# Kernel optimization log

Measured on AMD Instinct MI355X. Metric: run time of the kernel, lower is better.

The kernel has to match this reference:

```python
import jax, jax.numpy as jnp
import numpy as np

EPS_NORM = 1e-12
EPS_ABS = 1e-12


def _stack3(x):
    # x: [B, T, C] -> [B, T, 3, C] with left-shift, identity, right-shift taps
    prev = jnp.pad(x[:, :-1, :], ((0, 0), (1, 0), (0, 0)))
    nxt = jnp.pad(x[:, 1:, :], ((0, 0), (0, 1), (0, 0)))
    return jnp.stack([prev, x, nxt], axis=2)


def _l2_norm(x, axis):
    # matches layer's l2_normal: sqrt(max(sum(x^2), eps)), keepdims
    sq = jnp.sum(jnp.square(x), axis=axis, keepdims=True)
    return jnp.sqrt(jnp.maximum(sq, EPS_NORM))


def setup_inputs() -> dict:
    key = jax.random.key(0)
    k1, k2 = jax.random.split(key)
    B, T, C, K, U = 32, 4096, 128, 3, 256
    inputs = jax.random.normal(k1, (B, T, C), dtype=jnp.float32)
    # glorot uniform for w: limit = sqrt(6/(fan_in+fan_out)) with fan_in=C*K, fan_out=U
    limit = np.sqrt(6.0 / (C * K + U)).astype(np.float32)
    w = jax.random.uniform(k2, (1, C * K, U), dtype=jnp.float32, minval=-limit, maxval=limit)
    b = jnp.zeros((U,), dtype=jnp.float32)
    p = jnp.ones((U,), dtype=jnp.float32)
    q = jnp.zeros((1,), dtype=jnp.float32)
    return {"inputs": inputs, "w": w, "b": b, "p": p, "q": q}


def reference(inputs, w, b, p, q):
    B, T, C = inputs.shape
    U = w.shape[-1]
    x = _stack3(inputs).reshape(B, T, 3 * C)          # [B, T, 3C] (tap-major, matches tf stack+reshape)
    q2 = jnp.square(q)                                 # [1]
    x_norm = _l2_norm(x, axis=2) + q2                  # [B, T, 1]
    w_norm = _l2_norm(w, axis=1) + q2                  # [1, 1, U]
    w2 = w[0]                                          # [3C, U]
    sign = jnp.sign(jnp.einsum('btk,ku->btu', x, w2))  # sign of raw matmul
    y = jnp.einsum('btk,ku->btu', x / x_norm, w2 / w_norm[0])
    y = jnp.abs(y) + EPS_ABS
    y = jnp.power(y, jnp.square(p))                    # broadcast over units
    y = sign * y + b
    return y
```

## Files before the change

kernel.cpp:

```cpp
#include <hip/hip_runtime.h>

typedef __attribute__((ext_vector_type(8))) short short8;
typedef __attribute__((ext_vector_type(4))) float f32x4;

#define T_DIM 4096
#define C_DIM 128
#define U_DIM 256
#define BM 128
#define NROWS 130
#define LDK 136

__device__ __forceinline__ unsigned short f2bf(float f) {
    unsigned int u = __float_as_uint(f);
    u += 0x7FFFu + ((u >> 16) & 1u);
    return (unsigned short)(u >> 16);
}

__global__ void prep_kernel(const float* __restrict__ w,
                            const float* __restrict__ b,
                            const float* __restrict__ p,
                            const float* __restrict__ q,
                            unsigned short* __restrict__ wfrag,
                            float* __restrict__ winv,
                            float* __restrict__ p2,
                            float* __restrict__ bc) {
    if (blockIdx.x < 48) {
        int idx = blockIdx.x * 256 + threadIdx.x;
        int l  = idx & 63;
        int nt = (idx >> 6) & 15;
        int ks = idx >> 10;
        int n  = nt * 16 + (l & 15);
        int k0 = ks * 32 + ((l >> 4) << 3);
        #pragma unroll
        for (int j = 0; j < 8; ++j) {
            wfrag[(size_t)idx * 8 + j] = f2bf(w[(k0 + j) * U_DIM + n]);
        }
    } else {
        int u = threadIdx.x;
        float ss = 0.f;
        for (int k = 0; k < 3 * C_DIM; ++k) {
            float v = w[k * U_DIM + u];
            ss += v * v;
        }
        float q2 = q[0] * q[0];
        winv[u] = 1.0f / (sqrtf(fmaxf(ss, 1e-12f)) + q2);
        float pv = p[u];
        p2[u] = pv * pv;
        bc[u] = b[u];
    }
}

__global__ __launch_bounds__(512, 4) void cossim_main(
        const float* __restrict__ inp,
        const unsigned short* __restrict__ wfrag,
        const float* __restrict__ winv,
        const float* __restrict__ p2g,
        const float* __restrict__ bg,
        const float* __restrict__ qg,
        float* __restrict__ out) {
    __shared__ unsigned short inp_s[NROWS][LDK];
    __shared__ float ss_s[NROWS];
    __shared__ float xninv_s[BM];

    const int tid  = threadIdx.x;
    const int bidx = blockIdx.x;
    const int bb   = bidx >> 5;
    const int t0   = (bidx & 31) * BM;

    {
        const int r0 = tid >> 5;
        const int lc = (tid & 31) * 4;
        float4 v[9];
        #pragma unroll
        for (int i = 0; i < 9; ++i) {
            int r = r0 + i * 16;
            int t = t0 + r - 1;
            float4 val = make_float4(0.f, 0.f, 0.f, 0.f);
            if (r < NROWS && t >= 0 && t < T_DIM) {
                val = *(const float4*)(inp + ((size_t)bb * T_DIM + t) * C_DIM + lc);
            }
            v[i] = val;
        }
        #pragma unroll
        for (int i = 0; i < 9; ++i) {
            int r = r0 + i * 16;
            if (r < NROWS) {
                float4 val = v[i];
                float part = val.x * val.x + val.y * val.y + val.z * val.z + val.w * val.w;
                #pragma unroll
                for (int o = 16; o > 0; o >>= 1) part += __shfl_xor(part, o, 32);
                if ((tid & 31) == 0) ss_s[r] = part;
                ushort4 sv;
                sv.x = f2bf(val.x); sv.y = f2bf(val.y);
                sv.z = f2bf(val.z); sv.w = f2bf(val.w);
                *(ushort4*)(&inp_s[r][lc]) = sv;
            }
        }
    }
    __syncthreads();
    if (tid < BM) {
        float s3 = ss_s[tid] + ss_s[tid + 1] + ss_s[tid + 2];
        float q2 = qg[0] * qg[0];
        xninv_s[tid] = 1.0f / (sqrtf(fmaxf(s3, 1e-12f)) + q2);
    }
    __syncthreads();

    const int wid = tid >> 6;
    const int l   = tid & 63;
    const int tw  = wid >> 2;
    const int uw  = wid & 3;
    const int l15 = l & 15;
    const int lg  = l >> 4;

    f32x4 acc[4][4];
    #pragma unroll
    for (int tf = 0; tf < 4; ++tf)
        #pragma unroll
        for (int uf = 0; uf < 4; ++uf)
            acc[tf][uf] = (f32x4){0.f, 0.f, 0.f, 0.f};

    const short8* wf = (const short8*)wfrag;

    #pragma unroll
    for (int ks = 0; ks < 12; ++ks) {
        const int tap = ks >> 2;
        const int c0  = (ks & 3) * 32 + lg * 8;
        short8 xv[4], wv[4];
        #pragma unroll
        for (int tf = 0; tf < 4; ++tf) {
            int row = tw * 64 + tf * 16 + l15 + tap;
            xv[tf] = *(const short8*)(&inp_s[row][c0]);
        }
        #pragma unroll
        for (int uf = 0; uf < 4; ++uf) {
            wv[uf] = wf[(size_t)(ks * 16 + uw * 4 + uf) * 64 + l];
        }
        #pragma unroll
        for (int tf = 0; tf < 4; ++tf)
            #pragma unroll
            for (int uf = 0; uf < 4; ++uf)
                acc[tf][uf] = __builtin_amdgcn_mfma_f32_16x16x32_bf16(
                    wv[uf], xv[tf], acc[tf][uf], 0, 0, 0);
    }

    #pragma unroll
    for (int tf = 0; tf < 4; ++tf) {
        int trow = tw * 64 + tf * 16 + l15;
        float xi = xninv_s[trow];
        float* orow = out + ((size_t)bb * T_DIM + t0 + trow) * U_DIM;
        #pragma unroll
        for (int uf = 0; uf < 4; ++uf) {
            int uc = uw * 64 + uf * 16 + lg * 4;
            f32x4 wiv = *(const f32x4*)(winv + uc);
            f32x4 ppv = *(const f32x4*)(p2g + uc);
            f32x4 bbv = *(const f32x4*)(bg + uc);
            f32x4 r;
            #pragma unroll
            for (int j = 0; j < 4; ++j) {
                float raw = acc[tf][uf][j];
                float y   = raw * xi * wiv[j];
                float ay  = fabsf(y) + 1e-12f;
                float pw  = ppv[j];
                float rr  = ay;
                if (pw != 1.0f) rr = powf(ay, pw);
                float s   = (raw > 0.f) ? 1.f : ((raw < 0.f) ? -1.f : 0.f);
                r[j] = s * rr + bbv[j];
            }
            *(f32x4*)(orow + uc) = r;
        }
    }
}

extern "C" void kernel_launch(void* const* d_in, const int* in_sizes, int n_in,
                              void* d_out, int out_size, void* d_ws, size_t ws_size,
                              hipStream_t stream) {
    const float* inp = (const float*)d_in[0];
    const float* w   = (const float*)d_in[1];
    const float* b   = (const float*)d_in[2];
    const float* p   = (const float*)d_in[3];
    const float* q   = (const float*)d_in[4];
    float* out = (float*)d_out;

    unsigned short* wfrag = (unsigned short*)d_ws;
    float* winv = (float*)((char*)d_ws + 196608);
    float* p2   = winv + 256;
    float* bc   = p2 + 256;

    prep_kernel<<<49, 256, 0, stream>>>(w, b, p, q, wfrag, winv, p2, bc);
    cossim_main<<<1024, 512, 0, stream>>>(inp, wfrag, winv, p2, bc, q, out);
}
```

Baseline: 74.01 us.

## Loop over multiple time tiles per block with register-prefetched double-buffered LDS

Each block now processes four 64-row time tiles sequentially instead of one 128-row tile. The next tile's input is loaded into registers during the current tile's MFMA and epilogue, then written to a second LDS buffer. The goal is to overlap global input loads with compute and output stores. In exchange, the grid is halved, halo overhead per tile rises, and the extra barriers add cost.

```diff
diff --git a/kernel.cpp b/kernel.cpp
--- a/kernel.cpp
+++ b/kernel.cpp
@@ -6,9 +6,10 @@
 #define T_DIM 4096
 #define C_DIM 128
 #define U_DIM 256
-#define BM 128
-#define NROWS 130
+#define BM 64
+#define NROWS 66
 #define LDK 136
+#define NT 4
 
 __device__ __forceinline__ unsigned short f2bf(float f) {
     unsigned int u = __float_as_uint(f);
@@ -58,52 +59,15 @@
         const float* __restrict__ bg,
         const float* __restrict__ qg,
         float* __restrict__ out) {
-    __shared__ unsigned short inp_s[NROWS][LDK];
-    __shared__ float ss_s[NROWS];
-    __shared__ float xninv_s[BM];
-
-    const int tid  = threadIdx.x;
-    const int bidx = blockIdx.x;
-    const int bb   = bidx >> 5;
-    const int t0   = (bidx & 31) * BM;
-
-    {
-        const int r0 = tid >> 5;
-        const int lc = (tid & 31) * 4;
-        float4 v[9];
-        #pragma unroll
-        for (int i = 0; i < 9; ++i) {
-            int r = r0 + i * 16;
-            int t = t0 + r - 1;
-            float4 val = make_float4(0.f, 0.f, 0.f, 0.f);
-            if (r < NROWS && t >= 0 && t < T_DIM) {
-                val = *(const float4*)(inp + ((size_t)bb * T_DIM + t) * C_DIM + lc);
-            }
-            v[i] = val;
-        }
-        #pragma unroll
-        for (int i = 0; i < 9; ++i) {
-            int r = r0 + i * 16;
-            if (r < NROWS) {
-                float4 val = v[i];
-                float part = val.x * val.x + val.y * val.y + val.z * val.z + val.w * val.w;
-                #pragma unroll
-                for (int o = 16; o > 0; o >>= 1) part += __shfl_xor(part, o, 32);
-                if ((tid & 31) == 0) ss_s[r] = part;
-                ushort4 sv;
-                sv.x = f2bf(val.x); sv.y = f2bf(val.y);
-                sv.z = f2bf(val.z); sv.w = f2bf(val.w);
-                *(ushort4*)(&inp_s[r][lc]) = sv;
-            }
-        }
-    }
-    __syncthreads();
-    if (tid < BM) {
-        float s3 = ss_s[tid] + ss_s[tid + 1] + ss_s[tid + 2];
-        float q2 = qg[0] * qg[0];
-        xninv_s[tid] = 1.0f / (sqrtf(fmaxf(s3, 1e-12f)) + q2);
-    }
-    __syncthreads();
+    __shared__ unsigned short xs[2][NROWS][LDK];
+    __shared__ float ss_s[2][NROWS];
+
+    const int tid = threadIdx.x;
+    const int bb  = blockIdx.x >> 4;
+    const int tp0 = (blockIdx.x & 15) * NT;
+
+    const int r0 = tid >> 5;
+    const int lc = (tid & 31) * 4;
 
     const int wid = tid >> 6;
     const int l   = tid & 63;
@@ -112,62 +76,139 @@
     const int l15 = l & 15;
     const int lg  = l >> 4;
 
-    f32x4 acc[4][4];
-    #pragma unroll
-    for (int tf = 0; tf < 4; ++tf)
-        #pragma unroll
-        for (int uf = 0; uf < 4; ++uf)
-            acc[tf][uf] = (f32x4){0.f, 0.f, 0.f, 0.f};
-
+    const float q2 = qg[0] * qg[0];
     const short8* wf = (const short8*)wfrag;
 
-    #pragma unroll
-    for (int ks = 0; ks < 12; ++ks) {
-        const int tap = ks >> 2;
-        const int c0  = (ks & 3) * 32 + lg * 8;
-        short8 xv[4], wv[4];
-        #pragma unroll
-        for (int tf = 0; tf < 4; ++tf) {
-            int row = tw * 64 + tf * 16 + l15 + tap;
-            xv[tf] = *(const short8*)(&inp_s[row][c0]);
-        }
-        #pragma unroll
-        for (int uf = 0; uf < 4; ++uf) {
-            wv[uf] = wf[(size_t)(ks * 16 + uw * 4 + uf) * 64 + l];
-        }
-        #pragma unroll
-        for (int tf = 0; tf < 4; ++tf)
+    float4 v[5];
+    {
+        const float* base = inp + (size_t)bb * T_DIM * C_DIM;
+        int t0 = tp0 * BM;
+        #pragma unroll
+        for (int jj = 0; jj < 5; ++jj) {
+            int r = r0 + jj * 16;
+            int t = t0 + r - 1;
+            float4 val = make_float4(0.f, 0.f, 0.f, 0.f);
+            if (r < NROWS && (unsigned)t < T_DIM)
+                val = *(const float4*)(base + (size_t)t * C_DIM + lc);
+            v[jj] = val;
+        }
+        #pragma unroll
+        for (int jj = 0; jj < 5; ++jj) {
+            int r = r0 + jj * 16;
+            if (r < NROWS) {
+                float4 val = v[jj];
+                float part = val.x * val.x + val.y * val.y + val.z * val.z + val.w * val.w;
+                #pragma unroll
+                for (int o = 16; o > 0; o >>= 1) part += __shfl_xor(part, o, 32);
+                if ((tid & 31) == 0) ss_s[0][r] = part;
+                ushort4 sv;
+                sv.x = f2bf(val.x); sv.y = f2bf(val.y);
+                sv.z = f2bf(val.z); sv.w = f2bf(val.w);
+                *(ushort4*)(&xs[0][r][lc]) = sv;
+            }
+        }
+    }
+    __syncthreads();
+
+    int cur = 0;
+    for (int i = 0; i < NT; ++i) {
+        const int t0 = (tp0 + i) * BM;
+
+        float4 vn[5];
+        if (i + 1 < NT) {
+            const float* base = inp + (size_t)bb * T_DIM * C_DIM;
+            int t0n = (tp0 + i + 1) * BM;
+            #pragma unroll
+            for (int jj = 0; jj < 5; ++jj) {
+                int r = r0 + jj * 16;
+                int t = t0n + r - 1;
+                float4 val = make_float4(0.f, 0.f, 0.f, 0.f);
+                if (r < NROWS && (unsigned)t < T_DIM)
+                    val = *(const float4*)(base + (size_t)t * C_DIM + lc);
+                vn[jj] = val;
+            }
+        }
+
+        const unsigned short (*xb)[LDK] = xs[cur];
+        const float* ssb = ss_s[cur];
+
+        f32x4 acc[2][4];
+        #pragma unroll
+        for (int tf = 0; tf < 2; ++tf)
             #pragma unroll
             for (int uf = 0; uf < 4; ++uf)
-                acc[tf][uf] = __builtin_amdgcn_mfma_f32_16x16x32_bf16(
-                    wv[uf], xv[tf], acc[tf][uf], 0, 0, 0);
-    }
-
-    #pragma unroll
-    for (int tf = 0; tf < 4; ++tf) {
-        int trow = tw * 64 + tf * 16 + l15;
-        float xi = xninv_s[trow];
-        float* orow = out + ((size_t)bb * T_DIM + t0 + trow) * U_DIM;
-        #pragma unroll
-        for (int uf = 0; uf < 4; ++uf) {
-            int uc = uw * 64 + uf * 16 + lg * 4;
-            f32x4 wiv = *(const f32x4*)(winv + uc);
-            f32x4 ppv = *(const f32x4*)(p2g + uc);
-            f32x4 bbv = *(const f32x4*)(bg + uc);
-            f32x4 r;
-            #pragma unroll
-            for (int j = 0; j < 4; ++j) {
-                float raw = acc[tf][uf][j];
-                float y   = raw * xi * wiv[j];
-                float ay  = fabsf(y) + 1e-12f;
-                float pw  = ppv[j];
-                float rr  = ay;
-                if (pw != 1.0f) rr = powf(ay, pw);
-                float s   = (raw > 0.f) ? 1.f : ((raw < 0.f) ? -1.f : 0.f);
-                r[j] = s * rr + bbv[j];
-            }
-            *(f32x4*)(orow + uc) = r;
-        }
+                acc[tf][uf] = (f32x4){0.f, 0.f, 0.f, 0.f};
+
+        #pragma unroll
+        for (int ks = 0; ks < 12; ++ks) {
+            const int tap = ks >> 2;
+            const int c0  = (ks & 3) * 32 + lg * 8;
+            short8 xv[2], wv[4];
+            #pragma unroll
+            for (int tf = 0; tf < 2; ++tf) {
+                int row = tw * 32 + tf * 16 + l15 + tap;
+                xv[tf] = *(const short8*)(&xb[row][c0]);
+            }
+            #pragma unroll
+            for (int uf = 0; uf < 4; ++uf) {
+                wv[uf] = wf[(size_t)(ks * 16 + uw * 4 + uf) * 64 + l];
+            }
+            #pragma unroll
+            for (int tf = 0; tf < 2; ++tf)
+                #pragma unroll
+                for (int uf = 0; uf < 4; ++uf)
+                    acc[tf][uf] = __builtin_amdgcn_mfma_f32_16x16x32_bf16(
+                        wv[uf], xv[tf], acc[tf][uf], 0, 0, 0);
+        }
+
+        #pragma unroll
+        for (int tf = 0; tf < 2; ++tf) {
+            int trow = tw * 32 + tf * 16 + l15;
+            float s3 = ssb[trow] + ssb[trow + 1] + ssb[trow + 2];
+            float xi = 1.0f / (sqrtf(fmaxf(s3, 1e-12f)) + q2);
+            float* orow = out + ((size_t)bb * T_DIM + t0 + trow) * U_DIM;
+            #pragma unroll
+            for (int uf = 0; uf < 4; ++uf) {
+                int uc = uw * 64 + uf * 16 + lg * 4;
+                f32x4 wiv = *(const f32x4*)(winv + uc);
+                f32x4 ppv = *(const f32x4*)(p2g + uc);
+                f32x4 bbv = *(const f32x4*)(bg + uc);
+                f32x4 r;
+                #pragma unroll
+                for (int j = 0; j < 4; ++j) {
+                    float raw = acc[tf][uf][j];
+                    float y   = raw * xi * wiv[j];
+                    float ay  = fabsf(y) + 1e-12f;
+                    float pw  = ppv[j];
+                    float rr  = ay;
+                    if (pw != 1.0f) rr = powf(ay, pw);
+                    float s   = (raw > 0.f) ? 1.f : ((raw < 0.f) ? -1.f : 0.f);
+                    r[j] = s * rr + bbv[j];
+                }
+                *(f32x4*)(orow + uc) = r;
+            }
+        }
+
+        if (i + 1 < NT) {
+            __syncthreads();
+            #pragma unroll
+            for (int jj = 0; jj < 5; ++jj) {
+                int r = r0 + jj * 16;
+                if (r < NROWS) {
+                    float4 val = vn[jj];
+                    float part = val.x * val.x + val.y * val.y + val.z * val.z + val.w * val.w;
+                    #pragma unroll
+                    for (int o = 16; o > 0; o >>= 1) part += __shfl_xor(part, o, 32);
+                    if ((tid & 31) == 0) ss_s[cur ^ 1][r] = part;
+                    ushort4 sv;
+                    sv.x = f2bf(val.x); sv.y = f2bf(val.y);
+                    sv.z = f2bf(val.z); sv.w = f2bf(val.w);
+                    *(ushort4*)(&xs[cur ^ 1][r][lc]) = sv;
+                }
+            }
+            __syncthreads();
+        }
+        cur ^= 1;
     }
 }
 
@@ -187,5 +228,5 @@
     float* bc   = p2 + 256;
 
     prep_kernel<<<49, 256, 0, stream>>>(w, b, p, q, wfrag, winv, p2, bc);
-    cossim_main<<<1024, 512, 0, stream>>>(inp, wfrag, winv, p2, bc, q, out);
-}
+    cossim_main<<<512, 512, 0, stream>>>(inp, wfrag, winv, p2, bc, q, out);
+}
```

Measured after the change: 285.2 us. +285.3%, slower.
